# Performance work log

Hardware: AMD Instinct MI355X
Metric: run time of the kernel (lower is better)

The kernel has to match this reference:

```python
import jax, jax.numpy as jnp
import numpy as np

INPUT_SIZE = 256
HIDDEN = 512
NUM_GRIDS = 512
BATCH = 256


def setup_inputs() -> dict:
    key = jax.random.key(0)
    ks = jax.random.split(key, 12)
    s_ih = 1.0 / np.sqrt(HIDDEN)
    inp = {
        "input_data": jax.random.normal(ks[0], (NUM_GRIDS, BATCH, INPUT_SIZE), dtype=jnp.float32),
        "h0": jax.random.normal(ks[1], (BATCH, HIDDEN), dtype=jnp.float32),
        "c0": jax.random.normal(ks[2], (BATCH, HIDDEN), dtype=jnp.float32),
        # LSTMCell params (PyTorch layout: [4H, in] with gate order i,f,g,o)
        "W_ih": jax.random.uniform(ks[3], (4 * HIDDEN, INPUT_SIZE), jnp.float32, -s_ih, s_ih),
        "W_hh": jax.random.uniform(ks[4], (4 * HIDDEN, HIDDEN), jnp.float32, -s_ih, s_ih),
        "b_ih": jax.random.uniform(ks[5], (4 * HIDDEN,), jnp.float32, -s_ih, s_ih),
        "b_hh": jax.random.uniform(ks[6], (4 * HIDDEN,), jnp.float32, -s_ih, s_ih),
        # dense heads
        "W1": jax.random.uniform(ks[7], (5, HIDDEN), jnp.float32, -s_ih, s_ih),
        "b1": jax.random.uniform(ks[8], (5,), jnp.float32, -s_ih, s_ih),
        "W2": jax.random.uniform(ks[9], (1, 5), jnp.float32, -0.44, 0.44),
        "b2": jax.random.uniform(ks[10], (1,), jnp.float32, -0.44, 0.44),
    }
    return inp


def reference(input_data, h0, c0, W_ih, W_hh, b_ih, b_hh, W1, b1, W2, b2):
    def step(carry, x_t):
        h, c = carry
        # gates: [B, 4H]
        gates = x_t @ W_ih.T + b_ih + h @ W_hh.T + b_hh
        i, f, g, o = jnp.split(gates, 4, axis=-1)
        i = jax.nn.sigmoid(i)
        f = jax.nn.sigmoid(f)
        g = jnp.tanh(g)
        o = jax.nn.sigmoid(o)
        c = f * c + i * g
        h = o * jnp.tanh(c)
        # small dense head + ELU per timestep
        y = jax.nn.elu((h @ W1.T + b1) @ W2.T + b2)  # [B, 1]
        return (h, c), y

    _, ys = jax.lax.scan(step, (h0, c0), input_data)  # ys: [T, B, 1]
    return ys
```

## Files before the change

### kernel.cpp

```cpp
#include <hip/hip_runtime.h>
#include <hip/hip_bf16.h>
#include <cstddef>


#define T_STEPS 512
#define BATCH 256
#define ISZ 256
#define HID 512
#define KTOT 768
#define KT_STEPS 24
#define AP 776

typedef _Float16 half8 __attribute__((ext_vector_type(8)));
typedef float f32x4 __attribute__((ext_vector_type(4)));

#define WS_XH    0
#define WS_WP    67108864
#define WS_BSUM  70254592
#define WS_HB0   70262784
#define WS_HB1   70524928
#define WS_C     70787072

__global__ void k_convX(const float* __restrict__ X, _Float16* __restrict__ Xh) {
    const size_t n4 = (size_t)T_STEPS * BATCH * ISZ / 4;
    for (size_t i = (size_t)blockIdx.x * blockDim.x + threadIdx.x; i < n4;
         i += (size_t)gridDim.x * blockDim.x) {
        float4 v = ((const float4*)X)[i];
        _Float16 h4[4] = {(_Float16)v.x, (_Float16)v.y, (_Float16)v.z, (_Float16)v.w};
        *(uint2*)(Xh + i * 4) = *(const uint2*)h4;
    }
}

__global__ void k_pack(const float* __restrict__ Wih, const float* __restrict__ Whh,
                       _Float16* __restrict__ Wp) {
    int idx = blockIdx.x * 256 + threadIdx.x;
    if (idx >= KTOT * 2048) return;
    int i    = idx & 7;
    int lane = (idx >> 3) & 63;
    int tile = idx >> 9;
    int kt = tile % KT_STEPS;
    int nt = tile / KT_STEPS;
    int n = nt * 16 + (lane & 15);
    int k = kt * 32 + (lane >> 4) * 8 + i;
    float v = (k < ISZ) ? Wih[n * ISZ + k] : Whh[n * HID + (k - ISZ)];
    Wp[idx] = (_Float16)v;
}

__global__ void k_misc(const float* __restrict__ bih, const float* __restrict__ bhh,
                       float* __restrict__ bsum, const float* __restrict__ h0,
                       _Float16* __restrict__ hb, const float* __restrict__ c0,
                       float* __restrict__ cst) {
    int idx = blockIdx.x * 256 + threadIdx.x;
    if (idx < 4 * HID) bsum[idx] = bih[idx] + bhh[idx];
    hb[idx] = (_Float16)h0[idx];
    cst[idx] = c0[idx];
}

__device__ __forceinline__ float sigm(float x) { return 1.f / (1.f + __expf(-x)); }
__device__ __forceinline__ float tanh_fast(float x) { return 2.f / (1.f + __expf(-2.f * x)) - 1.f; }

__global__ __launch_bounds__(256) void k_step(
    const _Float16* __restrict__ Xh, const _Float16* __restrict__ Wp,
    const float* __restrict__ bsum,
    const _Float16* __restrict__ hprev, _Float16* __restrict__ hnext,
    float* __restrict__ cst,
    const float* __restrict__ W1, const float* __restrict__ b1,
    const float* __restrict__ W2, const float* __restrict__ b2,
    float* __restrict__ out, int t)
{
    __shared__ _Float16 A[32 * AP];
    __shared__ float yp[32 * 8 * 5];

    const int tid = threadIdx.x;
    const int blk = blockIdx.x;
    const int bt = blk >> 4, jt = blk & 15;
    const int b0 = bt * 32, j0 = jt * 32;

    #pragma unroll
    for (int it = 0; it < 12; ++it) {
        int cid = tid + it * 256;
        if (cid < 1024) {
            int r = cid >> 5, kh = (cid & 31) * 8;
            uint4 v = *(const uint4*)(Xh + ((size_t)t * BATCH + b0 + r) * ISZ + kh);
            *(uint4*)&A[r * AP + kh] = v;
        } else {
            int c2 = cid - 1024;
            int r = c2 >> 6, kh = (c2 & 63) * 8;
            uint4 v = *(const uint4*)(hprev + (size_t)(b0 + r) * HID + kh);
            *(uint4*)&A[r * AP + ISZ + kh] = v;
        }
    }
    __syncthreads();

    if (jt == 0 && t > 0) {
        int row = tid >> 3, seg = tid & 7;
        float p[5] = {0.f, 0.f, 0.f, 0.f, 0.f};
        int kbase = seg * 64;
        for (int k = kbase; k < kbase + 64; ++k) {
            float hv = (float)A[row * AP + ISZ + k];
            #pragma unroll
            for (int m = 0; m < 5; ++m) p[m] += hv * W1[m * HID + k];
        }
        #pragma unroll
        for (int m = 0; m < 5; ++m) yp[(row * 8 + seg) * 5 + m] = p[m];
    }
    __syncthreads();
    if (jt == 0 && t > 0 && tid < 32) {
        float z = b2[0];
        #pragma unroll
        for (int m = 0; m < 5; ++m) {
            float am = b1[m];
            for (int s = 0; s < 8; ++s) am += yp[(tid * 8 + s) * 5 + m];
            z += am * W2[m];
        }
        out[(size_t)(t - 1) * BATCH + b0 + tid] = z > 0.f ? z : (__expf(z) - 1.f);
    }

    const int wave = tid >> 6, lane = tid & 63;
    const int jw = j0 + (wave & 1) * 16;
    const int mh = wave >> 1;
    const int ar = mh * 16 + (lane & 15);
    const int kg = (lane >> 4) * 8;

    f32x4 acc[4];
    #pragma unroll
    for (int g = 0; g < 4; ++g) acc[g] = (f32x4){0.f, 0.f, 0.f, 0.f};

    int ntg[4];
    #pragma unroll
    for (int g = 0; g < 4; ++g) ntg[g] = g * 32 + (jw >> 4);

    for (int kt = 0; kt < KT_STEPS; ++kt) {
        half8 a = *(const half8*)&A[ar * AP + kt * 32 + kg];
        #pragma unroll
        for (int g = 0; g < 4; ++g) {
            half8 b = *(const half8*)(Wp + ((size_t)(ntg[g] * KT_STEPS + kt) << 9) + lane * 8);
            acc[g] = __builtin_amdgcn_mfma_f32_16x16x32_f16(a, b, acc[g], 0, 0, 0);
        }
    }

    const int col = lane & 15;
    const int j = jw + col;
    const int rbase = b0 + mh * 16 + ((lane >> 4) << 2);
    const float bi = bsum[j], bf = bsum[HID + j], bg = bsum[2 * HID + j], bo = bsum[3 * HID + j];
    #pragma unroll
    for (int i2 = 0; i2 < 4; ++i2) {
        int r = rbase + i2;
        float gi = acc[0][i2] + bi;
        float gf = acc[1][i2] + bf;
        float gg = acc[2][i2] + bg;
        float go = acc[3][i2] + bo;
        float si = sigm(gi), sf = sigm(gf), tg = tanh_fast(gg), so = sigm(go);
        size_t ci = (size_t)r * HID + j;
        float cn = sf * cst[ci] + si * tg;
        cst[ci] = cn;
        hnext[ci] = (_Float16)(so * tanh_fast(cn));
    }
}

__global__ __launch_bounds__(256) void k_ytail(
    const _Float16* __restrict__ h, const float* __restrict__ W1,
    const float* __restrict__ b1, const float* __restrict__ W2,
    const float* __restrict__ b2, float* __restrict__ out)
{
    __shared__ float yp[32 * 8 * 5];
    const int tid = threadIdx.x;
    const int b0 = blockIdx.x * 32;
    int row = tid >> 3, seg = tid & 7;
    float p[5] = {0.f, 0.f, 0.f, 0.f, 0.f};
    int kbase = seg * 64;
    for (int k = kbase; k < kbase + 64; ++k) {
        float hv = (float)h[(size_t)(b0 + row) * HID + k];
        #pragma unroll
        for (int m = 0; m < 5; ++m) p[m] += hv * W1[m * HID + k];
    }
    #pragma unroll
    for (int m = 0; m < 5; ++m) yp[(row * 8 + seg) * 5 + m] = p[m];
    __syncthreads();
    if (tid < 32) {
        float z = b2[0];
        #pragma unroll
        for (int m = 0; m < 5; ++m) {
            float am = b1[m];
            for (int s = 0; s < 8; ++s) am += yp[(tid * 8 + s) * 5 + m];
            z += am * W2[m];
        }
        out[(size_t)(T_STEPS - 1) * BATCH + b0 + tid] = z > 0.f ? z : (__expf(z) - 1.f);
    }
}

extern "C" void kernel_launch(void* const* d_in, const int* in_sizes, int n_in,
                              void* d_out, int out_size, void* d_ws, size_t ws_size,
                              hipStream_t stream) {
    const float* X   = (const float*)d_in[0];
    const float* h0  = (const float*)d_in[1];
    const float* c0  = (const float*)d_in[2];
    const float* Wih = (const float*)d_in[3];
    const float* Whh = (const float*)d_in[4];
    const float* bih = (const float*)d_in[5];
    const float* bhh = (const float*)d_in[6];
    const float* W1  = (const float*)d_in[7];
    const float* b1  = (const float*)d_in[8];
    const float* W2  = (const float*)d_in[9];
    const float* b2  = (const float*)d_in[10];
    float* out = (float*)d_out;

    char* ws = (char*)d_ws;
    _Float16* Xh   = (_Float16*)(ws + WS_XH);
    _Float16* Wp   = (_Float16*)(ws + WS_WP);
    float*    bsum = (float*)(ws + WS_BSUM);
    _Float16* hb0  = (_Float16*)(ws + WS_HB0);
    _Float16* hb1  = (_Float16*)(ws + WS_HB1);
    float*    cst  = (float*)(ws + WS_C);

    k_convX<<<2048, 256, 0, stream>>>(X, Xh);
    k_pack<<<(KTOT * 2048 + 255) / 256, 256, 0, stream>>>(Wih, Whh, Wp);
    k_misc<<<512, 256, 0, stream>>>(bih, bhh, bsum, h0, hb0, c0, cst);

    for (int t = 0; t < T_STEPS; ++t) {
        const _Float16* hp = (t & 1) ? hb1 : hb0;
        _Float16*       hn = (t & 1) ? hb0 : hb1;
        k_step<<<128, 256, 0, stream>>>(Xh, Wp, bsum, hp, hn, cst,
                                        W1, b1, W2, b2, out, t);
    }
    k_ytail<<<8, 256, 0, stream>>>(hb0, W1, b1, W2, b2, out);
}
```

Before: 8.450 ms.

## Fuse all LSTM timesteps into one persistent kernel with grid barriers

Replaces the 512 per-timestep kernel launches with a single persistent kernel of 256 blocks that loops over time and synchronises through an atomic-counter grid barrier. Each wave keeps its weight fragments in registers for the whole run, and each thread keeps its cell state in registers, so neither is re-read from global memory every step. The gate combine goes through shared memory. The barrier relies on all 256 blocks being co-resident and has a spin cap that could silently break ordering if it is exceeded.

Result: slower. 27.96 ms (+230.9%).

```diff
diff --git a/kernel.cpp b/kernel.cpp
--- a/kernel.cpp
+++ b/kernel.cpp
@@ -1,6 +1,7 @@
 #include <hip/hip_runtime.h>
 #include <hip/hip_bf16.h>
 #include <cstddef>
+#include <cstdint>
 
 
 #define T_STEPS 512
@@ -10,16 +11,17 @@
 #define KTOT 768
 #define KT_STEPS 24
 #define AP 776
+#define NBLK 256
+#define SPIN_CAP 200000
 
 typedef _Float16 half8 __attribute__((ext_vector_type(8)));
 typedef float f32x4 __attribute__((ext_vector_type(4)));
 
 #define WS_XH    0
 #define WS_WP    67108864
-#define WS_BSUM  70254592
-#define WS_HB0   70262784
-#define WS_HB1   70524928
-#define WS_C     70787072
+#define WS_HB0   70254592
+#define WS_HB1   70516736
+#define WS_CNT   70778880
 
 __global__ void k_convX(const float* __restrict__ X, _Float16* __restrict__ Xh) {
     const size_t n4 = (size_t)T_STEPS * BATCH * ISZ / 4;
@@ -46,146 +48,161 @@
     Wp[idx] = (_Float16)v;
 }
 
-__global__ void k_misc(const float* __restrict__ bih, const float* __restrict__ bhh,
-                       float* __restrict__ bsum, const float* __restrict__ h0,
-                       _Float16* __restrict__ hb, const float* __restrict__ c0,
-                       float* __restrict__ cst) {
+__global__ void k_inith(const float* __restrict__ h0, _Float16* __restrict__ hb,
+                        unsigned int* __restrict__ cnt) {
     int idx = blockIdx.x * 256 + threadIdx.x;
-    if (idx < 4 * HID) bsum[idx] = bih[idx] + bhh[idx];
+    if (threadIdx.x == 0) *cnt = 0u;
     hb[idx] = (_Float16)h0[idx];
-    cst[idx] = c0[idx];
 }
 
 __device__ __forceinline__ float sigm(float x) { return 1.f / (1.f + __expf(-x)); }
 __device__ __forceinline__ float tanh_fast(float x) { return 2.f / (1.f + __expf(-2.f * x)) - 1.f; }
 
-__global__ __launch_bounds__(256) void k_step(
+__device__ __forceinline__ void grid_barrier(unsigned int* cnt, unsigned int target) {
+    __threadfence();
+    __syncthreads();
+    if (threadIdx.x == 0) {
+        __hip_atomic_fetch_add(cnt, 1u, __ATOMIC_RELEASE, __HIP_MEMORY_SCOPE_AGENT);
+        unsigned int polls = 0;
+        while (__hip_atomic_load(cnt, __ATOMIC_ACQUIRE, __HIP_MEMORY_SCOPE_AGENT) < target
+               && ++polls < SPIN_CAP)
+            __builtin_amdgcn_s_sleep(1);
+    }
+    __syncthreads();
+    __threadfence();
+}
+
+__global__ __launch_bounds__(256, 1) void k_lstm(
     const _Float16* __restrict__ Xh, const _Float16* __restrict__ Wp,
-    const float* __restrict__ bsum,
-    const _Float16* __restrict__ hprev, _Float16* __restrict__ hnext,
-    float* __restrict__ cst,
+    const float* __restrict__ bih, const float* __restrict__ bhh,
+    _Float16* hb0, _Float16* hb1,
+    const float* __restrict__ c0,
     const float* __restrict__ W1, const float* __restrict__ b1,
     const float* __restrict__ W2, const float* __restrict__ b2,
-    float* __restrict__ out, int t)
+    float* __restrict__ out, unsigned int* __restrict__ cnt)
 {
     __shared__ _Float16 A[32 * AP];
+    __shared__ float gbuf[32 * 68];
+    __shared__ float w1s[5 * HID];
     __shared__ float yp[32 * 8 * 5];
 
     const int tid = threadIdx.x;
     const int blk = blockIdx.x;
-    const int bt = blk >> 4, jt = blk & 15;
-    const int b0 = bt * 32, j0 = jt * 32;
-
+    const int bt = blk >> 5, jt = blk & 31;
+    const int b0 = bt * 32, j0 = jt * 16;
+    const int wave = tid >> 6, lane = tid & 63;
+
+    const int nt = wave * 32 + jt;
+    half8 bfrag[KT_STEPS];
     #pragma unroll
-    for (int it = 0; it < 12; ++it) {
-        int cid = tid + it * 256;
-        if (cid < 1024) {
-            int r = cid >> 5, kh = (cid & 31) * 8;
-            uint4 v = *(const uint4*)(Xh + ((size_t)t * BATCH + b0 + r) * ISZ + kh);
-            *(uint4*)&A[r * AP + kh] = v;
-        } else {
-            int c2 = cid - 1024;
-            int r = c2 >> 6, kh = (c2 & 63) * 8;
-            uint4 v = *(const uint4*)(hprev + (size_t)(b0 + r) * HID + kh);
-            *(uint4*)&A[r * AP + ISZ + kh] = v;
-        }
-    }
-    __syncthreads();
-
-    if (jt == 0 && t > 0) {
-        int row = tid >> 3, seg = tid & 7;
-        float p[5] = {0.f, 0.f, 0.f, 0.f, 0.f};
-        int kbase = seg * 64;
-        for (int k = kbase; k < kbase + 64; ++k) {
-            float hv = (float)A[row * AP + ISZ + k];
-            #pragma unroll
-            for (int m = 0; m < 5; ++m) p[m] += hv * W1[m * HID + k];
-        }
+    for (int kt = 0; kt < KT_STEPS; ++kt)
+        bfrag[kt] = *(const half8*)(Wp + ((size_t)(nt * KT_STEPS + kt) << 9) + lane * 8);
+
+    const int erow = (tid * 2) >> 4;
+    const int ecol = (tid * 2) & 15;
+    float bias[2][4];
+    float creg[2];
+    #pragma unroll
+    for (int e = 0; e < 2; ++e) {
+        int j = j0 + ecol + e;
         #pragma unroll
-        for (int m = 0; m < 5; ++m) yp[(row * 8 + seg) * 5 + m] = p[m];
-    }
-    __syncthreads();
-    if (jt == 0 && t > 0 && tid < 32) {
-        float z = b2[0];
+        for (int g = 0; g < 4; ++g)
+            bias[e][g] = bih[g * HID + j] + bhh[g * HID + j];
+        creg[e] = c0[(size_t)(b0 + erow) * HID + j];
+    }
+
+    float w2r[5] = {0,0,0,0,0}, b1r[5] = {0,0,0,0,0}, b2r = 0.f;
+    if (jt == 0) {
+        for (int i = tid; i < 5 * HID; i += 256) w1s[i] = W1[i];
         #pragma unroll
-        for (int m = 0; m < 5; ++m) {
-            float am = b1[m];
-            for (int s = 0; s < 8; ++s) am += yp[(tid * 8 + s) * 5 + m];
-            z += am * W2[m];
-        }
-        out[(size_t)(t - 1) * BATCH + b0 + tid] = z > 0.f ? z : (__expf(z) - 1.f);
-    }
-
-    const int wave = tid >> 6, lane = tid & 63;
-    const int jw = j0 + (wave & 1) * 16;
-    const int mh = wave >> 1;
-    const int ar = mh * 16 + (lane & 15);
-    const int kg = (lane >> 4) * 8;
-
-    f32x4 acc[4];
-    #pragma unroll
-    for (int g = 0; g < 4; ++g) acc[g] = (f32x4){0.f, 0.f, 0.f, 0.f};
-
-    int ntg[4];
-    #pragma unroll
-    for (int g = 0; g < 4; ++g) ntg[g] = g * 32 + (jw >> 4);
-
-    for (int kt = 0; kt < KT_STEPS; ++kt) {
-        half8 a = *(const half8*)&A[ar * AP + kt * 32 + kg];
+        for (int m = 0; m < 5; ++m) { w2r[m] = W2[m]; b1r[m] = b1[m]; }
+        b2r = b2[0];
+    }
+
+    for (int t = 0; t <= T_STEPS; ++t) {
+        const _Float16* hprev = (t & 1) ? hb1 : hb0;
+        _Float16*       hnext = (t & 1) ? hb0 : hb1;
+
         #pragma unroll
-        for (int g = 0; g < 4; ++g) {
-            half8 b = *(const half8*)(Wp + ((size_t)(ntg[g] * KT_STEPS + kt) << 9) + lane * 8);
-            acc[g] = __builtin_amdgcn_mfma_f32_16x16x32_f16(a, b, acc[g], 0, 0, 0);
-        }
-    }
-
-    const int col = lane & 15;
-    const int j = jw + col;
-    const int rbase = b0 + mh * 16 + ((lane >> 4) << 2);
-    const float bi = bsum[j], bf = bsum[HID + j], bg = bsum[2 * HID + j], bo = bsum[3 * HID + j];
-    #pragma unroll
-    for (int i2 = 0; i2 < 4; ++i2) {
-        int r = rbase + i2;
-        float gi = acc[0][i2] + bi;
-        float gf = acc[1][i2] + bf;
-        float gg = acc[2][i2] + bg;
-        float go = acc[3][i2] + bo;
-        float si = sigm(gi), sf = sigm(gf), tg = tanh_fast(gg), so = sigm(go);
-        size_t ci = (size_t)r * HID + j;
-        float cn = sf * cst[ci] + si * tg;
-        cst[ci] = cn;
-        hnext[ci] = (_Float16)(so * tanh_fast(cn));
-    }
-}
-
-__global__ __launch_bounds__(256) void k_ytail(
-    const _Float16* __restrict__ h, const float* __restrict__ W1,
-    const float* __restrict__ b1, const float* __restrict__ W2,
-    const float* __restrict__ b2, float* __restrict__ out)
-{
-    __shared__ float yp[32 * 8 * 5];
-    const int tid = threadIdx.x;
-    const int b0 = blockIdx.x * 32;
-    int row = tid >> 3, seg = tid & 7;
-    float p[5] = {0.f, 0.f, 0.f, 0.f, 0.f};
-    int kbase = seg * 64;
-    for (int k = kbase; k < kbase + 64; ++k) {
-        float hv = (float)h[(size_t)(b0 + row) * HID + k];
-        #pragma unroll
-        for (int m = 0; m < 5; ++m) p[m] += hv * W1[m * HID + k];
-    }
-    #pragma unroll
-    for (int m = 0; m < 5; ++m) yp[(row * 8 + seg) * 5 + m] = p[m];
-    __syncthreads();
-    if (tid < 32) {
-        float z = b2[0];
-        #pragma unroll
-        for (int m = 0; m < 5; ++m) {
-            float am = b1[m];
-            for (int s = 0; s < 8; ++s) am += yp[(tid * 8 + s) * 5 + m];
-            z += am * W2[m];
-        }
-        out[(size_t)(T_STEPS - 1) * BATCH + b0 + tid] = z > 0.f ? z : (__expf(z) - 1.f);
+        for (int it = 0; it < 12; ++it) {
+            int cid = tid + it * 256;
+            if (cid < 1024) {
+                if (t < T_STEPS) {
+                    int r = cid >> 5, kh = (cid & 31) * 8;
+                    *(uint4*)&A[r * AP + kh] =
+                        *(const uint4*)(Xh + ((size_t)t * BATCH + b0 + r) * ISZ + kh);
+                }
+            } else {
+                int c2 = cid - 1024;
+                int r = c2 >> 6, kh = (c2 & 63) * 8;
+                *(uint4*)&A[r * AP + ISZ + kh] =
+                    *(const uint4*)(hprev + (size_t)(b0 + r) * HID + kh);
+            }
+        }
+        __syncthreads();
+
+        if (jt == 0 && t > 0) {
+            int row = tid >> 3, seg = tid & 7;
+            float p[5] = {0.f, 0.f, 0.f, 0.f, 0.f};
+            int kb = seg * 64;
+            for (int k = kb; k < kb + 64; ++k) {
+                float hv = (float)A[row * AP + ISZ + k];
+                #pragma unroll
+                for (int m = 0; m < 5; ++m) p[m] += hv * w1s[m * HID + k];
+            }
+            #pragma unroll
+            for (int m = 0; m < 5; ++m) yp[(row * 8 + seg) * 5 + m] = p[m];
+        }
+
+        if (t < T_STEPS) {
+            f32x4 acc0 = {0.f, 0.f, 0.f, 0.f}, acc1 = {0.f, 0.f, 0.f, 0.f};
+            const int ar0 = (lane & 15) * AP + (lane >> 4) * 8;
+            #pragma unroll
+            for (int kt = 0; kt < KT_STEPS; ++kt) {
+                half8 a0 = *(const half8*)&A[ar0 + kt * 32];
+                half8 a1 = *(const half8*)&A[ar0 + 16 * AP + kt * 32];
+                acc0 = __builtin_amdgcn_mfma_f32_16x16x32_f16(a0, bfrag[kt], acc0, 0, 0, 0);
+                acc1 = __builtin_amdgcn_mfma_f32_16x16x32_f16(a1, bfrag[kt], acc1, 0, 0, 0);
+            }
+            {
+                int col = lane & 15, r4 = (lane >> 4) * 4;
+                #pragma unroll
+                for (int i = 0; i < 4; ++i) {
+                    gbuf[(r4 + i) * 68 + wave * 16 + col]      = acc0[i];
+                    gbuf[(16 + r4 + i) * 68 + wave * 16 + col] = acc1[i];
+                }
+            }
+        }
+        __syncthreads();
+
+        if (jt == 0 && t > 0 && tid < 32) {
+            float z = b2r;
+            #pragma unroll
+            for (int m = 0; m < 5; ++m) {
+                float am = b1r[m];
+                for (int s = 0; s < 8; ++s) am += yp[(tid * 8 + s) * 5 + m];
+                z += am * w2r[m];
+            }
+            out[(size_t)(t - 1) * BATCH + b0 + tid] = z > 0.f ? z : (__expf(z) - 1.f);
+        }
+
+        if (t < T_STEPS) {
+            union { _Float16 h[2]; uint32_t u; } hu;
+            #pragma unroll
+            for (int e = 0; e < 2; ++e) {
+                int col = ecol + e;
+                float gi = gbuf[erow * 68 + 0 * 16 + col] + bias[e][0];
+                float gf = gbuf[erow * 68 + 1 * 16 + col] + bias[e][1];
+                float gg = gbuf[erow * 68 + 2 * 16 + col] + bias[e][2];
+                float go = gbuf[erow * 68 + 3 * 16 + col] + bias[e][3];
+                float si = sigm(gi), sf = sigm(gf), tg = tanh_fast(gg), so = sigm(go);
+                float cn = sf * creg[e] + si * tg;
+                creg[e] = cn;
+                hu.h[e] = (_Float16)(so * tanh_fast(cn));
+            }
+            *(uint32_t*)(hnext + (size_t)(b0 + erow) * HID + j0 + ecol) = hu.u;
+            grid_barrier(cnt, (unsigned int)(t + 1) * NBLK);
+        }
     }
 }
 
@@ -206,22 +223,16 @@
     float* out = (float*)d_out;
 
     char* ws = (char*)d_ws;
-    _Float16* Xh   = (_Float16*)(ws + WS_XH);
-    _Float16* Wp   = (_Float16*)(ws + WS_WP);
-    float*    bsum = (float*)(ws + WS_BSUM);
-    _Float16* hb0  = (_Float16*)(ws + WS_HB0);
-    _Float16* hb1  = (_Float16*)(ws + WS_HB1);
-    float*    cst  = (float*)(ws + WS_C);
+    _Float16* Xh  = (_Float16*)(ws + WS_XH);
+    _Float16* Wp  = (_Float16*)(ws + WS_WP);
+    _Float16* hb0 = (_Float16*)(ws + WS_HB0);
+    _Float16* hb1 = (_Float16*)(ws + WS_HB1);
+    unsigned int* cnt = (unsigned int*)(ws + WS_CNT);
 
     k_convX<<<2048, 256, 0, stream>>>(X, Xh);
     k_pack<<<(KTOT * 2048 + 255) / 256, 256, 0, stream>>>(Wih, Whh, Wp);
-    k_misc<<<512, 256, 0, stream>>>(bih, bhh, bsum, h0, hb0, c0, cst);
-
-    for (int t = 0; t < T_STEPS; ++t) {
-        const _Float16* hp = (t & 1) ? hb1 : hb0;
-        _Float16*       hn = (t & 1) ? hb0 : hb1;
-        k_step<<<128, 256, 0, stream>>>(Xh, Wp, bsum, hp, hn, cst,
-                                        W1, b1, W2, b2, out, t);
-    }
-    k_ytail<<<8, 256, 0, stream>>>(hb0, W1, b1, W2, b2, out);
-}
+    k_inith<<<512, 256, 0, stream>>>(h0, hb0, cnt);
+
+    k_lstm<<<NBLK, 256, 0, stream>>>(Xh, Wp, bih, bhh, hb0, hb1, c0,
+                                     W1, b1, W2, b2, out, cnt);
+}
```
